# Performance work log

Measured on AMD Instinct MI355X. Metric: run time of the kernel, lower is better.

## Reference

```python
import jax, jax.numpy as jnp
import numpy as np

EPS = 1e-5


def setup_inputs() -> dict:
    key = jax.random.key(0)
    ks = jax.random.split(key, 8)
    g, p, d, h, w = 32, 64, 512, 24, 8
    hw = h * w
    return {
        "gal_fea": jax.random.normal(ks[0], (g, d, h, w), dtype=jnp.float32),
        "prob_fea": jax.random.normal(ks[1], (p, d, h, w), dtype=jnp.float32),
        "bn_weight": jnp.ones((1,), jnp.float32),
        "bn_bias": jnp.zeros((1,), jnp.float32),
        "bn_mean": jax.random.normal(ks[2], (1,), jnp.float32) * 0.1,
        "bn_var": jax.random.uniform(ks[3], (1,), jnp.float32, 0.5, 1.5),
        "fc_weight": jax.random.normal(ks[4], (1, 2 * hw), jnp.float32) * 0.05,
        "fc_bias": jnp.zeros((1,), jnp.float32),
        "lbn_weight": jnp.ones((1,), jnp.float32),
        "lbn_bias": jnp.zeros((1,), jnp.float32),
        "lbn_mean": jax.random.normal(ks[5], (1,), jnp.float32) * 0.1,
        "lbn_var": jax.random.uniform(ks[6], (1,), jnp.float32, 0.5, 1.5),
    }


def reference(gal_fea, prob_fea, bn_weight, bn_bias, bn_mean, bn_var,
              fc_weight, fc_bias, lbn_weight, lbn_bias, lbn_mean, lbn_var):
    g, d, h, w = gal_fea.shape
    p = prob_fea.shape[0]
    hw = h * w
    # 1x1 conv with probe pixels as kernels == batched correlation (QK^T style)
    gal = gal_fea.reshape(g, d, hw)                                  # [g, d, hw_x]
    ker = jnp.transpose(prob_fea, (0, 2, 3, 1)).reshape(p, hw, d)    # [p, hw_y, d]
    s = jnp.einsum('gdx,pyd->gpyx', gal, ker)                        # [g, p, hw_y, hw_x]
    # dual-axis max pooling, then concat: [g, p, 2*hw]
    score = jnp.concatenate([s.max(axis=2), s.max(axis=3)], axis=-1)
    # BatchNorm1d(1) in eval mode: scalar affine with running stats
    score = (score - bn_mean) * (bn_weight / jnp.sqrt(bn_var + EPS)) + bn_bias
    # fc: Linear(2*hw, 1)
    score = score.reshape(g * p, 2 * hw) @ fc_weight[0] + fc_bias[0]  # [g*p]
    score = score.reshape(g, p)
    # logit BatchNorm1d(1), eval mode
    score = (score - lbn_mean) * (lbn_weight / jnp.sqrt(lbn_var + EPS)) + lbn_bias
    return jax.nn.sigmoid(score / 10.0)
```

## Files before the change

### kernel.cpp

```cpp
#include <hip/hip_runtime.h>
#include <hip/hip_bf16.h>
#include <cstdint>
#include <cstddef>

#define NG 32
#define NP 64
#define ND 512
#define HW 192
#define KS 32
#define EPSV 1e-5f

typedef _Float16 half8 __attribute__((ext_vector_type(8)));
typedef float floatx4 __attribute__((ext_vector_type(4)));
typedef float floatx16 __attribute__((ext_vector_type(16)));

__global__ __launch_bounds__(256) void prep_frag(const float* __restrict__ gal,
                                                 const float* __restrict__ prob,
                                                 _Float16* __restrict__ galT4,
                                                 _Float16* __restrict__ probT4) {
  __shared__ float lds[16 * 192];
  const int z = blockIdx.x;
  const int ks = blockIdx.y;
  const float* src;
  _Float16* dst;
  if (z < NP) {
    src = prob + (size_t)z * ND * HW;
    dst = probT4 + (size_t)z * 98304;
  } else {
    src = gal + (size_t)(z - NP) * ND * HW;
    dst = galT4 + (size_t)(z - NP) * 98304;
  }
  src += (size_t)ks * 16 * HW;
  dst += (size_t)ks * 3072;
  const int t = threadIdx.x;
#pragma unroll
  for (int i = 0; i < 12; ++i) lds[i * 256 + t] = src[i * 256 + t];
  __syncthreads();
#pragma unroll
  for (int r = 0; r < 2; ++r) {
    const int h = r * 256 + t;
    if (h < 384) {
      const int rb = h >> 6, hi = (h >> 5) & 1, l31 = h & 31;
      half8 v;
#pragma unroll
      for (int j = 0; j < 8; ++j) v[j] = (_Float16)lds[(hi * 8 + j) * 192 + rb * 32 + l31];
      *(half8*)(dst + (size_t)h * 8) = v;
    }
  }
}

__global__ __launch_bounds__(256, 2) void qaconv_main(
    const _Float16* __restrict__ galT4, const _Float16* __restrict__ probT4,
    const float* __restrict__ bn_w, const float* __restrict__ bn_b,
    const float* __restrict__ bn_m, const float* __restrict__ bn_v,
    const float* __restrict__ fc_w, const float* __restrict__ fc_b,
    const float* __restrict__ lbn_w, const float* __restrict__ lbn_b,
    const float* __restrict__ lbn_m, const float* __restrict__ lbn_v,
    float* __restrict__ out) {
  __shared__ float colp[2][HW];
  __shared__ float rowpart[2][HW];
  __shared__ float wsum[4];

  const int bid = blockIdx.x;
  const int g = bid >> 6, p = bid & 63;

  const int t = threadIdx.x;
  const int lane = t & 63, wid = t >> 6;
  const int wr = wid & 1;
  const int wc = wid >> 1;
  const int l31 = lane & 31, hi = lane >> 5;

  const _Float16* pA = probT4 + (size_t)p * 98304 + wr * 1536 + lane * 8;
  const _Float16* pB = galT4 + (size_t)g * 98304 + wc * 1536 + lane * 8;

  floatx16 acc[3][3];
#pragma unroll
  for (int ii = 0; ii < 3; ++ii)
#pragma unroll
    for (int jj = 0; jj < 3; ++jj) acc[ii][jj] = (floatx16)0.f;

#define LOADF(AF, BF, ks_)                                   \
  {                                                          \
    const _Float16* a_ = pA + (size_t)(ks_)*3072;            \
    const _Float16* b_ = pB + (size_t)(ks_)*3072;            \
    AF[0] = *(const half8*)(a_);                             \
    AF[1] = *(const half8*)(a_ + 512);                       \
    AF[2] = *(const half8*)(a_ + 1024);                      \
    BF[0] = *(const half8*)(b_);                             \
    BF[1] = *(const half8*)(b_ + 512);                       \
    BF[2] = *(const half8*)(b_ + 1024);                      \
  }

#define MFMAS(AF, BF)                                                            \
  {                                                                              \
    __builtin_amdgcn_s_setprio(1);                                               \
    _Pragma("unroll") for (int ii = 0; ii < 3; ++ii)                             \
        _Pragma("unroll") for (int jj = 0; jj < 3; ++jj)                         \
            acc[ii][jj] = __builtin_amdgcn_mfma_f32_32x32x16_f16(AF[ii], BF[jj], \
                                                                 acc[ii][jj], 0, 0, 0); \
    __builtin_amdgcn_s_setprio(0);                                               \
  }

  half8 af0[3], bf0[3], af1[3], bf1[3];
  LOADF(af0, bf0, 0)
  LOADF(af1, bf1, 1)
  for (int ks = 0; ks < KS; ks += 2) {
    const int n0 = (ks + 2 < KS) ? ks + 2 : 30;
    const int n1 = (ks + 3 < KS) ? ks + 3 : 31;
    MFMAS(af0, bf0)
    LOADF(af0, bf0, n0)
    MFMAS(af1, bf1)
    LOADF(af1, bf1, n1)
  }

#pragma unroll
  for (int fb = 0; fb < 3; ++fb) {
    float v = -3.4e38f;
#pragma unroll
    for (int fa = 0; fa < 3; ++fa)
#pragma unroll
      for (int e = 0; e < 16; ++e) v = fmaxf(v, acc[fa][fb][e]);
    v = fmaxf(v, __shfl_xor(v, 32));
    if (lane < 32) colp[wr][wc * 96 + fb * 32 + lane] = v;
  }
#pragma unroll
  for (int fa = 0; fa < 3; ++fa)
#pragma unroll
    for (int e = 0; e < 16; ++e) {
      float rv = fmaxf(fmaxf(acc[fa][0][e], acc[fa][1][e]), acc[fa][2][e]);
      rv = fmaxf(rv, __shfl_xor(rv, 1));
      rv = fmaxf(rv, __shfl_xor(rv, 2));
      rv = fmaxf(rv, __shfl_xor(rv, 4));
      rv = fmaxf(rv, __shfl_xor(rv, 8));
      rv = fmaxf(rv, __shfl_xor(rv, 16));
      if (l31 == 0) {
        const int Y = wr * 96 + fa * 32 + (e & 3) + 8 * (e >> 2) + 4 * hi;
        rowpart[wc][Y] = rv;
      }
    }
  __syncthreads();

  float partial = 0.f;
  if (t < HW) {
    const float rmax = fmaxf(rowpart[0][t], rowpart[1][t]);
    const float cmax = fmaxf(colp[0][t], colp[1][t]);
    const float scale = bn_w[0] / sqrtf(bn_v[0] + EPSV);
    const float bm = bn_m[0], bb = bn_b[0];
    partial = ((cmax - bm) * scale + bb) * fc_w[t] +
              ((rmax - bm) * scale + bb) * fc_w[HW + t];
  }
#pragma unroll
  for (int off = 1; off < 64; off <<= 1) partial += __shfl_xor(partial, off);
  if (lane == 0) wsum[wid] = partial;
  __syncthreads();
  if (t == 0) {
    const float sum = fc_b[0] + wsum[0] + wsum[1] + wsum[2] + wsum[3];
    const float logit = (sum - lbn_m[0]) * (lbn_w[0] / sqrtf(lbn_v[0] + EPSV)) + lbn_b[0];
    out[bid] = 1.f / (1.f + expf(-logit * 0.1f));
  }
#undef LOADF
#undef MFMAS
}

__global__ __launch_bounds__(256) void qaconv_naive(
    const float* __restrict__ gal, const float* __restrict__ prob,
    const float* __restrict__ bn_w, const float* __restrict__ bn_b,
    const float* __restrict__ bn_m, const float* __restrict__ bn_v,
    const float* __restrict__ fc_w, const float* __restrict__ fc_b,
    const float* __restrict__ lbn_w, const float* __restrict__ lbn_b,
    const float* __restrict__ lbn_m, const float* __restrict__ lbn_v,
    float* __restrict__ out) {
  __shared__ float prow[ND];
  __shared__ float rowmaxs[HW];
  __shared__ float colmaxs[HW];
  __shared__ float red[4];
  const int bid = blockIdx.x;
  const int g = bid >> 6, p = bid & 63;
  const int t = threadIdx.x, lane = t & 63, wid = t >> 6;
  const float* gp = gal + (size_t)g * ND * HW;
  const float* pp = prob + (size_t)p * ND * HW;
  float colmax = -3.4e38f;
  for (int y = 0; y < HW; ++y) {
    for (int k = t; k < ND; k += 256) prow[k] = pp[(size_t)k * HW + y];
    __syncthreads();
    float sv = -3.4e38f;
    if (t < HW) {
      sv = 0.f;
      for (int k = 0; k < ND; ++k) sv = fmaf(prow[k], gp[(size_t)k * HW + t], sv);
      colmax = fmaxf(colmax, sv);
    }
    float m = sv;
#pragma unroll
    for (int off = 1; off < 64; off <<= 1) m = fmaxf(m, __shfl_xor(m, off));
    if (lane == 0) red[wid] = m;
    __syncthreads();
    if (t == 0) rowmaxs[y] = fmaxf(fmaxf(red[0], red[1]), fmaxf(red[2], red[3]));
    __syncthreads();
  }
  if (t < HW) colmaxs[t] = colmax;
  __syncthreads();
  float partial = 0.f;
  for (int j = t; j < 2 * HW; j += 256) {
    const float v = (j < HW) ? colmaxs[j] : rowmaxs[j - HW];
    const float sc = (v - bn_m[0]) * (bn_w[0] / sqrtf(bn_v[0] + EPSV)) + bn_b[0];
    partial += sc * fc_w[j];
  }
#pragma unroll
  for (int off = 1; off < 64; off <<= 1) partial += __shfl_xor(partial, off);
  if (lane == 0) red[wid] = partial;
  __syncthreads();
  if (t == 0) {
    const float sum = fc_b[0] + red[0] + red[1] + red[2] + red[3];
    const float logit = (sum - lbn_m[0]) * (lbn_w[0] / sqrtf(lbn_v[0] + EPSV)) + lbn_b[0];
    out[bid] = 1.f / (1.f + expf(-logit * 0.1f));
  }
}

extern "C" void kernel_launch(void* const* d_in, const int* in_sizes, int n_in,
                              void* d_out, int out_size, void* d_ws, size_t ws_size,
                              hipStream_t stream) {
  const float* gal = (const float*)d_in[0];
  const float* prob = (const float*)d_in[1];
  const float* bn_w = (const float*)d_in[2];
  const float* bn_b = (const float*)d_in[3];
  const float* bn_m = (const float*)d_in[4];
  const float* bn_v = (const float*)d_in[5];
  const float* fc_w = (const float*)d_in[6];
  const float* fc_b = (const float*)d_in[7];
  const float* lbn_w = (const float*)d_in[8];
  const float* lbn_b = (const float*)d_in[9];
  const float* lbn_m = (const float*)d_in[10];
  const float* lbn_v = (const float*)d_in[11];
  float* out = (float*)d_out;

  const size_t probT4_elems = (size_t)NP * 98304;
  const size_t galT4_elems = (size_t)NG * 98304;
  const size_t ws_needed = (probT4_elems + galT4_elems) * sizeof(_Float16);
  if (ws_size >= ws_needed) {
    _Float16* probT4 = (_Float16*)d_ws;
    _Float16* galT4 = probT4 + probT4_elems;
    prep_frag<<<dim3(NP + NG, KS), dim3(256), 0, stream>>>(gal, prob, galT4, probT4);
    qaconv_main<<<dim3(NG * NP), dim3(256), 0, stream>>>(
        galT4, probT4, bn_w, bn_b, bn_m, bn_v, fc_w, fc_b, lbn_w, lbn_b, lbn_m, lbn_v, out);
  } else {
    qaconv_naive<<<dim3(NG * NP), dim3(256), 0, stream>>>(
        gal, prob, bn_w, bn_b, bn_m, bn_v, fc_w, fc_b, lbn_w, lbn_b, lbn_m, lbn_v, out);
  }
}
```

Measured before the change: 109.2 us.

## Stage fragments through LDS with async global_load_lds and six-wave triple buffering

After: 158.6 us. +45.2%, slower.

```diff
diff --git a/kernel.cpp b/kernel.cpp
--- a/kernel.cpp
+++ b/kernel.cpp
@@ -49,7 +49,13 @@
   }
 }
 
-__global__ __launch_bounds__(256, 2) void qaconv_main(
+__device__ __forceinline__ void g2l16(const void* g, void* l) {
+  __builtin_amdgcn_global_load_lds(
+      (const __attribute__((address_space(1))) void*)g,
+      (__attribute__((address_space(3))) void*)l, 16, 0, 0);
+}
+
+__global__ __launch_bounds__(384, 3) void qaconv_main(
     const _Float16* __restrict__ galT4, const _Float16* __restrict__ probT4,
     const float* __restrict__ bn_w, const float* __restrict__ bn_b,
     const float* __restrict__ bn_m, const float* __restrict__ bn_v,
@@ -57,85 +63,133 @@
     const float* __restrict__ lbn_w, const float* __restrict__ lbn_b,
     const float* __restrict__ lbn_m, const float* __restrict__ lbn_v,
     float* __restrict__ out) {
-  __shared__ float colp[2][HW];
+  __shared__ __align__(16) char tiles[3][24576];
+  __shared__ float colp[3][HW];
   __shared__ float rowpart[2][HW];
-  __shared__ float wsum[4];
+  __shared__ float wsum[6];
 
   const int bid = blockIdx.x;
   const int g = bid >> 6, p = bid & 63;
 
   const int t = threadIdx.x;
   const int lane = t & 63, wid = t >> 6;
-  const int wr = wid & 1;
-  const int wc = wid >> 1;
+  const int wy = wid % 3;
+  const int wx = wid / 3;
   const int l31 = lane & 31, hi = lane >> 5;
 
-  const _Float16* pA = probT4 + (size_t)p * 98304 + wr * 1536 + lane * 8;
-  const _Float16* pB = galT4 + (size_t)g * 98304 + wc * 1536 + lane * 8;
-
-  floatx16 acc[3][3];
-#pragma unroll
-  for (int ii = 0; ii < 3; ++ii)
+  const _Float16* pAs = probT4 + (size_t)p * 98304 + (size_t)t * 8;
+  const _Float16* pBs = galT4 + (size_t)g * 98304 + (size_t)t * 8;
+
+  floatx16 acc[2][3];
+#pragma unroll
+  for (int ii = 0; ii < 2; ++ii)
 #pragma unroll
     for (int jj = 0; jj < 3; ++jj) acc[ii][jj] = (floatx16)0.f;
 
-#define LOADF(AF, BF, ks_)                                   \
-  {                                                          \
-    const _Float16* a_ = pA + (size_t)(ks_)*3072;            \
-    const _Float16* b_ = pB + (size_t)(ks_)*3072;            \
-    AF[0] = *(const half8*)(a_);                             \
-    AF[1] = *(const half8*)(a_ + 512);                       \
-    AF[2] = *(const half8*)(a_ + 1024);                      \
-    BF[0] = *(const half8*)(b_);                             \
-    BF[1] = *(const half8*)(b_ + 512);                       \
-    BF[2] = *(const half8*)(b_ + 1024);                      \
-  }
-
-#define MFMAS(AF, BF)                                                            \
+  half8 af[2], bf[3];
+
+#define STAGE(kt_, base_)                                            \
+  {                                                                  \
+    char* db_ = (char*)(base_) + t * 16;                             \
+    const _Float16* sa_ = pAs + (size_t)(kt_)*6144;                  \
+    const _Float16* sb_ = pBs + (size_t)(kt_)*6144;                  \
+    g2l16(sa_, db_);                                                 \
+    g2l16(sa_ + 3072, db_ + 6144);                                   \
+    g2l16(sb_, db_ + 12288);                                         \
+    g2l16(sb_ + 3072, db_ + 18432);                                  \
+  }
+
+#define READ5(base_, kc_)                                            \
+  {                                                                  \
+    const char* bA_ = (const char*)(base_) + (kc_)*6144;             \
+    const char* bB_ = (const char*)(base_) + 12288 + (kc_)*6144;     \
+    af[0] = *(const half8*)(bA_ + (wy * 2 + 0) * 1024 + lane * 16);  \
+    af[1] = *(const half8*)(bA_ + (wy * 2 + 1) * 1024 + lane * 16);  \
+    bf[0] = *(const half8*)(bB_ + (wx * 3 + 0) * 1024 + lane * 16);  \
+    bf[1] = *(const half8*)(bB_ + (wx * 3 + 1) * 1024 + lane * 16);  \
+    bf[2] = *(const half8*)(bB_ + (wx * 3 + 2) * 1024 + lane * 16);  \
+  }
+
+#define MFMA6()                                                                  \
   {                                                                              \
     __builtin_amdgcn_s_setprio(1);                                               \
-    _Pragma("unroll") for (int ii = 0; ii < 3; ++ii)                             \
+    _Pragma("unroll") for (int ii = 0; ii < 2; ++ii)                             \
         _Pragma("unroll") for (int jj = 0; jj < 3; ++jj)                         \
-            acc[ii][jj] = __builtin_amdgcn_mfma_f32_32x32x16_f16(AF[ii], BF[jj], \
+            acc[ii][jj] = __builtin_amdgcn_mfma_f32_32x32x16_f16(af[ii], bf[jj], \
                                                                  acc[ii][jj], 0, 0, 0); \
     __builtin_amdgcn_s_setprio(0);                                               \
   }
 
-  half8 af0[3], bf0[3], af1[3], bf1[3];
-  LOADF(af0, bf0, 0)
-  LOADF(af1, bf1, 1)
-  for (int ks = 0; ks < KS; ks += 2) {
-    const int n0 = (ks + 2 < KS) ? ks + 2 : 30;
-    const int n1 = (ks + 3 < KS) ? ks + 3 : 31;
-    MFMAS(af0, bf0)
-    LOADF(af0, bf0, n0)
-    MFMAS(af1, bf1)
-    LOADF(af1, bf1, n1)
-  }
-
-#pragma unroll
-  for (int fb = 0; fb < 3; ++fb) {
+#define SLOT(kt_, rdb_, stb_, doStage_, vmW_)                \
+  {                                                          \
+    READ5(rdb_, 0)                                           \
+    if (doStage_) STAGE((kt_) + 2, stb_)                     \
+    __builtin_amdgcn_sched_barrier(0);                       \
+    __builtin_amdgcn_s_barrier();                            \
+    asm volatile("s_waitcnt lgkmcnt(0)" ::: "memory");       \
+    __builtin_amdgcn_sched_barrier(0);                       \
+    MFMA6()                                                  \
+    __builtin_amdgcn_s_barrier();                            \
+    READ5(rdb_, 1)                                           \
+    __builtin_amdgcn_sched_barrier(0);                       \
+    asm volatile("s_waitcnt vmcnt(" #vmW_ ")" ::: "memory"); \
+    __builtin_amdgcn_s_barrier();                            \
+    asm volatile("s_waitcnt lgkmcnt(0)" ::: "memory");       \
+    __builtin_amdgcn_sched_barrier(0);                       \
+    MFMA6()                                                  \
+    __builtin_amdgcn_s_barrier();                            \
+  }
+
+  STAGE(0, tiles[0])
+  STAGE(1, tiles[1])
+  asm volatile("s_waitcnt vmcnt(4)" ::: "memory");
+  __builtin_amdgcn_s_barrier();
+
+#pragma unroll 1
+  for (int m = 0; m < 4; ++m) {
+    SLOT(3 * m + 0, tiles[0], tiles[2], true, 4)
+    SLOT(3 * m + 1, tiles[1], tiles[0], true, 4)
+    SLOT(3 * m + 2, tiles[2], tiles[1], true, 4)
+  }
+  SLOT(12, tiles[0], tiles[2], true, 4)
+  SLOT(13, tiles[1], tiles[0], true, 4)
+  SLOT(14, tiles[2], tiles[1], false, 0)
+  READ5(tiles[0], 0)
+  asm volatile("s_waitcnt lgkmcnt(0)" ::: "memory");
+  __builtin_amdgcn_sched_barrier(0);
+  MFMA6()
+  READ5(tiles[0], 1)
+  asm volatile("s_waitcnt lgkmcnt(0)" ::: "memory");
+  __builtin_amdgcn_sched_barrier(0);
+  MFMA6()
+#undef STAGE
+#undef READ5
+#undef MFMA6
+#undef SLOT
+
+#pragma unroll
+  for (int fx = 0; fx < 3; ++fx) {
     float v = -3.4e38f;
 #pragma unroll
-    for (int fa = 0; fa < 3; ++fa)
-#pragma unroll
-      for (int e = 0; e < 16; ++e) v = fmaxf(v, acc[fa][fb][e]);
+    for (int fy = 0; fy < 2; ++fy)
+#pragma unroll
+      for (int e = 0; e < 16; ++e) v = fmaxf(v, acc[fy][fx][e]);
     v = fmaxf(v, __shfl_xor(v, 32));
-    if (lane < 32) colp[wr][wc * 96 + fb * 32 + lane] = v;
-  }
-#pragma unroll
-  for (int fa = 0; fa < 3; ++fa)
+    if (lane < 32) colp[wy][wx * 96 + fx * 32 + lane] = v;
+  }
+#pragma unroll
+  for (int fy = 0; fy < 2; ++fy)
 #pragma unroll
     for (int e = 0; e < 16; ++e) {
-      float rv = fmaxf(fmaxf(acc[fa][0][e], acc[fa][1][e]), acc[fa][2][e]);
+      float rv = fmaxf(fmaxf(acc[fy][0][e], acc[fy][1][e]), acc[fy][2][e]);
       rv = fmaxf(rv, __shfl_xor(rv, 1));
       rv = fmaxf(rv, __shfl_xor(rv, 2));
       rv = fmaxf(rv, __shfl_xor(rv, 4));
       rv = fmaxf(rv, __shfl_xor(rv, 8));
       rv = fmaxf(rv, __shfl_xor(rv, 16));
       if (l31 == 0) {
-        const int Y = wr * 96 + fa * 32 + (e & 3) + 8 * (e >> 2) + 4 * hi;
-        rowpart[wc][Y] = rv;
+        const int Y = wy * 64 + fy * 32 + (e & 3) + 8 * (e >> 2) + 4 * hi;
+        rowpart[wx][Y] = rv;
       }
     }
   __syncthreads();
@@ -143,7 +197,7 @@
   float partial = 0.f;
   if (t < HW) {
     const float rmax = fmaxf(rowpart[0][t], rowpart[1][t]);
-    const float cmax = fmaxf(colp[0][t], colp[1][t]);
+    const float cmax = fmaxf(fmaxf(colp[0][t], colp[1][t]), colp[2][t]);
     const float scale = bn_w[0] / sqrtf(bn_v[0] + EPSV);
     const float bm = bn_m[0], bb = bn_b[0];
     partial = ((cmax - bm) * scale + bb) * fc_w[t] +
@@ -154,12 +208,12 @@
   if (lane == 0) wsum[wid] = partial;
   __syncthreads();
   if (t == 0) {
-    const float sum = fc_b[0] + wsum[0] + wsum[1] + wsum[2] + wsum[3];
+    float sum = fc_b[0];
+#pragma unroll
+    for (int w = 0; w < 6; ++w) sum += wsum[w];
     const float logit = (sum - lbn_m[0]) * (lbn_w[0] / sqrtf(lbn_v[0] + EPSV)) + lbn_b[0];
     out[bid] = 1.f / (1.f + expf(-logit * 0.1f));
   }
-#undef LOADF
-#undef MFMAS
 }
 
 __global__ __launch_bounds__(256) void qaconv_naive(
@@ -240,7 +294,7 @@
     _Float16* probT4 = (_Float16*)d_ws;
     _Float16* galT4 = probT4 + probT4_elems;
     prep_frag<<<dim3(NP + NG, KS), dim3(256), 0, stream>>>(gal, prob, galT4, probT4);
-    qaconv_main<<<dim3(NG * NP), dim3(256), 0, stream>>>(
+    qaconv_main<<<dim3(NG * NP), dim3(384), 0, stream>>>(
         galT4, probT4, bn_w, bn_b, bn_m, bn_v, fc_w, fc_b, lbn_w, lbn_b, lbn_m, lbn_v, out);
   } else {
     qaconv_naive<<<dim3(NG * NP), dim3(256), 0, stream>>>(
```
